# Kernel tuning notes

Measured on AMD Instinct MI355X. Metric: run time of the kernel, lower is better.

## Reference

```python
import jax, jax.numpy as jnp
import numpy as np

# Static configuration (mirrors init_kwargs)
B, C, H, W = 4, 256, 128, 128
S, T = 512, 64          # style_dim, num style tokens
HC, HS = 4, 8           # cross-attn heads, spatial-attn heads
WS, G = 8, 4            # window size, groupnorm groups
SHARPEN = 2.0
EPS = 1e-5


def _ln(x, g, b):
    m = jnp.mean(x, -1, keepdims=True)
    v = jnp.var(x, -1, keepdims=True)
    return (x - m) * jax.lax.rsqrt(v + EPS) * g + b


def _sdpa(q, k, v, scale):
    # q,k,v: [B, nH, L, D]
    s = jnp.einsum('bhqd,bhkd->bhqk', q, k) * scale
    return jnp.einsum('bhqk,bhkd->bhqd', jax.nn.softmax(s, -1), v)


def _heads(t, nh):
    b, l, c = t.shape
    return t.reshape(b, l, nh, c // nh).transpose(0, 2, 1, 3)


def _unheads(t):
    b, nh, l, d = t.shape
    return t.transpose(0, 2, 1, 3).reshape(b, l, nh * d)


def setup_inputs() -> dict:
    key = jax.random.key(0)
    ks = iter(jax.random.split(key, 48))
    def w(shape, s=0.02):
        return jax.random.normal(next(ks), shape, jnp.float32) * s
    return {
        'x': jax.random.normal(next(ks), (B, C, H, W), jnp.float32),
        'style_code': jax.random.normal(next(ks), (B, S), jnp.float32),
        # SpatialSelfAttention params (1x1 convs == linear over channels)
        'qkv_w': w((3 * C, C)), 'spat_proj_w': w((C, C)),
        # CrossAttnAdaGN params
        'gproj_w': w((2 * C, S)),
        'gproj_b': jnp.concatenate([jnp.ones((C,), jnp.float32), jnp.zeros((C,), jnp.float32)]),
        'tokens_basis': w((T, C)),
        'sproj_w': w((C, S)), 'sproj_b': jnp.zeros((C,), jnp.float32),
        'pos_w1': w((C, 2)), 'pos_b1': jnp.zeros((C,), jnp.float32),
        'pos_w2': w((C, C)), 'pos_b2': jnp.zeros((C,), jnp.float32),
        'q_w': w((C, C)), 'q_b': jnp.zeros((C,), jnp.float32),
        'k_w': w((C, C)), 'k_b': jnp.zeros((C,), jnp.float32),
        'v_w': w((C, C)), 'v_b': jnp.zeros((C,), jnp.float32),
        'o_w': w((C, C)), 'o_b': jnp.zeros((C,), jnp.float32),
        'ffn_w1': w((2 * C, C)), 'ffn_b1': jnp.zeros((2 * C,), jnp.float32),
        'ffn_w2': w((C, 2 * C)), 'ffn_b2': jnp.zeros((C,), jnp.float32),
        'tn_g': jnp.ones((C,), jnp.float32), 'tn_b': jnp.zeros((C,), jnp.float32),
        'qn_g': jnp.ones((C,), jnp.float32), 'qn_b': jnp.zeros((C,), jnp.float32),
        'fn_g': jnp.ones((C,), jnp.float32), 'fn_b': jnp.zeros((C,), jnp.float32),
        'gamma': w((1, C, 1, 1), 0.1),
    }


def reference(x, style_code, qkv_w, spat_proj_w, gproj_w, gproj_b, tokens_basis,
              sproj_w, sproj_b, pos_w1, pos_b1, pos_w2, pos_b2,
              q_w, q_b, k_w, k_b, v_w, v_b, o_w, o_b,
              ffn_w1, ffn_b1, ffn_w2, ffn_b2,
              tn_g, tn_b, qn_g, qn_b, fn_g, fn_b, gamma):
    b = x.shape[0]
    hw = H * W
    # ---------- CrossAttnAdaGN style modulation ----------
    xg = x.reshape(b, G, C // G, H, W)
    mu = jnp.mean(xg, (2, 3, 4), keepdims=True)
    var = jnp.var(xg, (2, 3, 4), keepdims=True)
    normalized = ((xg - mu) * jax.lax.rsqrt(var + EPS)).reshape(b, C, H, W)
    gp = style_code @ gproj_w.T + gproj_b           # [B, 2C]
    scale = gp[:, :C, None, None]
    shift = gp[:, C:, None, None]
    style_tokens = tokens_basis[None] + (style_code @ sproj_w.T + sproj_b)[:, None]  # [B,T,C]
    style_tokens = _ln(style_tokens, tn_g, tn_b)
    gy = jnp.linspace(-1.0, 1.0, H)
    gx = jnp.linspace(-1.0, 1.0, W)
    grid_y, grid_x = jnp.meshgrid(gy, gx, indexing='ij')
    pos = jnp.stack([grid_x, grid_y], -1).reshape(hw, 2)                 # [HW,2]
    pos_emb = jax.nn.silu(pos @ pos_w1.T + pos_b1) @ pos_w2.T + pos_b2   # [HW,C]
    tok = normalized.transpose(0, 2, 3, 1).reshape(b, hw, C)
    q_in = _ln(tok + pos_emb[None], qn_g, qn_b)
    q = _heads(q_in @ q_w.T + q_b, HC)                 # [B,HC,HW,hd]
    k = _heads(style_tokens @ k_w.T + k_b, HC)         # [B,HC,T,hd]
    v = _heads(style_tokens @ v_w.T + v_b, HC)
    hd = C // HC
    sc = _unheads(_sdpa(q, k, v, SHARPEN / jnp.sqrt(jnp.float32(hd))))   # [B,HW,C]
    sc = sc @ o_w.T + o_b
    sc = sc + jax.nn.silu(_ln(sc, fn_g, fn_b) @ ffn_w1.T + ffn_b1) @ ffn_w2.T + ffn_b2
    sc_sp = sc.transpose(0, 2, 1).reshape(b, C, H, W)
    adagn = normalized * scale + shift + sc_sp * gamma
    h = x + adagn  # gate = 1.0, residual style modulation
    # ---------- shifted-window self-attention ----------
    sh = WS // 2
    xr = jnp.roll(h, (-sh, -sh), (2, 3))
    qkv = jnp.einsum('oi,bihw->bohw', qkv_w, xr)
    qs, ks_, vs = jnp.split(qkv, 3, axis=1)
    def win(t):  # [B,C,H,W] -> [B*nWin, WS*WS, C]
        return t.reshape(b, C, H // WS, WS, W // WS, WS).transpose(0, 2, 4, 3, 5, 1).reshape(-1, WS * WS, C)
    hd2 = C // HS
    qh = _heads(win(qs), HS)
    kh = _heads(win(ks_), HS)
    vh = _heads(win(vs), HS)
    out = _unheads(_sdpa(qh, kh, vh, 1.0 / jnp.sqrt(jnp.float32(hd2))))
    out = out.reshape(b, H // WS, W // WS, WS, WS, C).transpose(0, 5, 1, 3, 2, 4).reshape(b, C, H, W)
    out = jnp.roll(out, (sh, sh), (2, 3))
    out = jnp.einsum('oi,bihw->bohw', spat_proj_w, out)
    return h + out
```

## Files before the change

### kernel.cpp

```cpp
#include <hip/hip_runtime.h>
#include <stdint.h>

#define DEV __device__ __forceinline__

typedef unsigned short u16;
typedef unsigned int u32;
typedef __attribute__((ext_vector_type(8))) __bf16 bf16x8;
typedef __attribute__((ext_vector_type(4))) float f32x4;

DEV u16 f2b(float f) {
  u32 u = __float_as_uint(f);
  u32 r = (u + 0x7FFFu + ((u >> 16) & 1u)) >> 16;
  return (u16)r;
}
DEV float b2f(u16 u) { return __uint_as_float(((u32)u) << 16); }
DEV void up2(u32 u, float& a, float& b) {
  a = __uint_as_float(u << 16);
  b = __uint_as_float(u & 0xffff0000u);
}
DEV void up8(uint4 t, float* d) {
  up2(t.x, d[0], d[1]); up2(t.y, d[2], d[3]);
  up2(t.z, d[4], d[5]); up2(t.w, d[6], d[7]);
}
DEV float silu_f(float v) { return v / (1.0f + __expf(-v)); }

DEV float redmax16(float v) {
  v = fmaxf(v, __shfl_xor(v, 1));
  v = fmaxf(v, __shfl_xor(v, 2));
  v = fmaxf(v, __shfl_xor(v, 4));
  v = fmaxf(v, __shfl_xor(v, 8));
  return v;
}
DEV float redsum16(float v) {
  v += __shfl_xor(v, 1);
  v += __shfl_xor(v, 2);
  v += __shfl_xor(v, 4);
  v += __shfl_xor(v, 8);
  return v;
}

__global__ void k_conv(const float* __restrict__ src, u16* __restrict__ dst, int n) {
  int i = blockIdx.x * 256 + threadIdx.x;
  int stride = gridDim.x * 256;
  for (; i < n; i += stride) dst[i] = f2b(src[i]);
}

DEV void breduce2(float& a, float& b, float* red, int tid) {
#pragma unroll
  for (int off = 32; off > 0; off >>= 1) {
    a += __shfl_down(a, off);
    b += __shfl_down(b, off);
  }
  int lane = tid & 63, wv = tid >> 6;
  if (lane == 0) { red[wv * 2] = a; red[wv * 2 + 1] = b; }
  __syncthreads();
  a = red[0] + red[2] + red[4] + red[6];
  b = red[1] + red[3] + red[5] + red[7];
}

__global__ void k_gn_partial(const float* __restrict__ x, float* __restrict__ partials) {
  __shared__ float red[8];
  int chunk = blockIdx.x;
  size_t base = ((size_t)chunk) << 14;
  float a = 0.f, b = 0.f;
#pragma unroll 4
  for (int i = 0; i < 64; ++i) {
    float v = x[base + (i << 8) + threadIdx.x];
    a += v; b += v * v;
  }
  breduce2(a, b, red, threadIdx.x);
  if (threadIdx.x == 0) { partials[chunk * 2] = a; partials[chunk * 2 + 1] = b; }
}

__global__ void k_gn_final(const float* __restrict__ partials, float* __restrict__ stats) {
  int g = blockIdx.x, lane = threadIdx.x;
  float a = partials[(((g << 6) + lane) << 1)];
  float b = partials[(((g << 6) + lane) << 1) + 1];
#pragma unroll
  for (int off = 32; off > 0; off >>= 1) {
    a += __shfl_down(a, off);
    b += __shfl_down(b, off);
  }
  if (lane == 0) {
    float mean = a * (1.f / 1048576.f);
    float var = b * (1.f / 1048576.f) - mean * mean;
    stats[g << 1] = mean;
    stats[(g << 1) + 1] = rsqrtf(var + 1e-5f);
  }
}

__global__ void k_style(const float* __restrict__ sc, const float* __restrict__ gw,
                        const float* __restrict__ gb, const float* __restrict__ sw,
                        const float* __restrict__ sb, float* __restrict__ gp,
                        float* __restrict__ stok) {
  __shared__ float row[512];
  int b = blockIdx.y, part = blockIdx.x, tid = threadIdx.x;
  row[tid] = sc[(b << 9) + tid];
  row[tid + 256] = sc[(b << 9) + tid + 256];
  __syncthreads();
  if (part < 2) {
    int o = (part << 8) + tid;
    float s = gb[o];
    const float* wr = gw + ((size_t)o << 9);
#pragma unroll 8
    for (int j = 0; j < 512; ++j) s += row[j] * wr[j];
    gp[(b << 9) + o] = s;
  } else {
    float s = sb[tid];
    const float* wr = sw + ((size_t)tid << 9);
#pragma unroll 8
    for (int j = 0; j < 512; ++j) s += row[j] * wr[j];
    stok[(b << 8) + tid] = s;
  }
}

__global__ void k_styk(const float* __restrict__ tb, const float* __restrict__ stok,
                       const float* __restrict__ g, const float* __restrict__ bt,
                       float* __restrict__ styk) {
  __shared__ float red[8];
  int r = blockIdx.x;
  int b = r >> 6, t = r & 63;
  int c = threadIdx.x;
  float v = tb[(t << 8) + c] + stok[(b << 8) + c];
  float a = v, bb = v * v;
  breduce2(a, bb, red, c);
  float mean = a * (1.f / 256.f);
  float var = bb * (1.f / 256.f) - mean * mean;
  float rs = rsqrtf(var + 1e-5f);
  styk[((size_t)r << 8) + c] = (v - mean) * rs * g[c] + bt[c];
}

__global__ void k_kv(const float* __restrict__ styk, const float* __restrict__ kw,
                     const float* __restrict__ kb, const float* __restrict__ vw,
                     const float* __restrict__ vb, u16* __restrict__ kmat,
                     u16* __restrict__ vmat) {
  __shared__ float srow[256];
  int r = blockIdx.x, c = threadIdx.x;
  srow[c] = styk[((size_t)r << 8) + c];
  __syncthreads();
  float sk = kb[c], sv = vb[c];
  const float* kr = kw + ((size_t)c << 8);
  const float* vr = vw + ((size_t)c << 8);
#pragma unroll 8
  for (int j = 0; j < 256; ++j) { sk += srow[j] * kr[j]; sv += srow[j] * vr[j]; }
  kmat[((size_t)r << 8) + c] = f2b(sk);
  vmat[((size_t)r << 8) + c] = f2b(sv);
}

__global__ void k_posh(const float* __restrict__ w1, const float* __restrict__ b1,
                       u16* __restrict__ posh) {
  int i = blockIdx.x * 256 + threadIdx.x;
  int stride = gridDim.x * 256;
  for (; i < 16384 * 256; i += stride) {
    int p = i >> 8, c = i & 255;
    int y = p >> 7, x = p & 127;
    float gx = -1.f + 2.f * (float)x / 127.f;
    float gy = -1.f + 2.f * (float)y / 127.f;
    float v = gx * w1[c << 1] + gy * w1[(c << 1) + 1] + b1[c];
    posh[i] = f2b(silu_f(v));
  }
}

template <int ACT, int BIAS, int RES, int OBF>
__global__ __launch_bounds__(256, 2) void k_gemm(
    const u16* __restrict__ A, const u16* __restrict__ Bw,
    const float* __restrict__ bias, const u16* __restrict__ res,
    void* __restrict__ outp, int M, int N, int K) {
  __shared__ u16 sA[128 * 40];
  __shared__ u16 sB[128 * 40];
  const int tid = threadIdx.x;
  const int m0 = blockIdx.y << 7, n0 = blockIdx.x << 7;
  const int lane = tid & 63, wv = tid >> 6;
  const int wr = wv >> 1, wc = wv & 1;
  const int l15 = lane & 15, kb = (lane >> 4) << 3;
  const int rA = (wr << 6) + l15, rB = (wc << 6) + l15;
  const int tr = tid >> 2, tc = (tid & 3) << 3;
  const u16* Ag = A + (size_t)(m0 + tr) * K + tc;
  const u16* Bg = Bw + (size_t)(n0 + tr) * K + tc;
  const size_t rowskip = (size_t)64 * K;

  f32x4 acc[4][4];
  f32x4 zz = {0.f, 0.f, 0.f, 0.f};
#pragma unroll
  for (int mi = 0; mi < 4; ++mi)
#pragma unroll
    for (int ni = 0; ni < 4; ++ni) acc[mi][ni] = zz;

  uint4 pa0 = *(const uint4*)(Ag);
  uint4 pa1 = *(const uint4*)(Ag + rowskip);
  uint4 pb0 = *(const uint4*)(Bg);
  uint4 pb1 = *(const uint4*)(Bg + rowskip);

  for (int k0 = 0; k0 < K; k0 += 32) {
    __syncthreads();
    *(uint4*)&sA[tr * 40 + tc] = pa0;
    *(uint4*)&sA[(tr + 64) * 40 + tc] = pa1;
    *(uint4*)&sB[tr * 40 + tc] = pb0;
    *(uint4*)&sB[(tr + 64) * 40 + tc] = pb1;
    __syncthreads();
    int kn = k0 + 32;
    if (kn < K) {
      pa0 = *(const uint4*)(Ag + kn);
      pa1 = *(const uint4*)(Ag + rowskip + kn);
      pb0 = *(const uint4*)(Bg + kn);
      pb1 = *(const uint4*)(Bg + rowskip + kn);
    }
    bf16x8 af[4], bfv[4];
#pragma unroll
    for (int i = 0; i < 4; ++i) {
      af[i] = *(const bf16x8*)&sA[(rA + (i << 4)) * 40 + kb];
      bfv[i] = *(const bf16x8*)&sB[(rB + (i << 4)) * 40 + kb];
    }
#pragma unroll
    for (int mi = 0; mi < 4; ++mi)
#pragma unroll
      for (int ni = 0; ni < 4; ++ni)
        acc[mi][ni] = __builtin_amdgcn_mfma_f32_16x16x32_bf16(af[mi], bfv[ni], acc[mi][ni], 0, 0, 0);
  }

  const int lg4 = (lane >> 4) << 2;
#pragma unroll
  for (int ni = 0; ni < 4; ++ni) {
    int n = n0 + (wc << 6) + (ni << 4) + l15;
    float bv = BIAS ? bias[n] : 0.0f;
#pragma unroll
    for (int mi = 0; mi < 4; ++mi) {
#pragma unroll
      for (int r = 0; r < 4; ++r) {
        int m = m0 + (wr << 6) + (mi << 4) + lg4 + r;
        float v = acc[mi][ni][r] + bv;
        if (ACT == 1) v = silu_f(v);
        size_t oi = (size_t)m * N + n;
        if (RES) v += b2f(res[oi]);
        if (OBF) ((u16*)outp)[oi] = f2b(v);
        else ((float*)outp)[oi] = v;
      }
    }
  }
}

__global__ void k_tokpe(const float* __restrict__ x, const float* __restrict__ stats,
                        const u16* __restrict__ pe, u16* __restrict__ tokq) {
  __shared__ float lds[64][65];
  int p0 = blockIdx.x << 6, c0 = blockIdx.y << 6, b = blockIdx.z;
  int tid = threadIdx.x;
#pragma unroll
  for (int i = 0; i < 16; ++i) {
    int flat = (i << 8) + tid;
    int ci = flat >> 6, pi = flat & 63;
    int cch = c0 + ci;
    int g = (b << 2) + (cch >> 6);
    float mu = stats[g << 1], rs = stats[(g << 1) + 1];
    lds[ci][pi] = (x[(((size_t)(b << 8) + cch) << 14) + p0 + pi] - mu) * rs;
  }
  __syncthreads();
#pragma unroll
  for (int i = 0; i < 16; ++i) {
    int flat = (i << 8) + tid;
    int pi = flat >> 6, ci = flat & 63;
    size_t row = (size_t)((b << 14) + p0 + pi);
    tokq[(row << 8) + c0 + ci] =
        f2b(lds[ci][pi] + b2f(pe[((size_t)(p0 + pi) << 8) + c0 + ci]));
  }
}

__global__ __launch_bounds__(256) void k_rowln8(const u16* __restrict__ in,
                                                const float* __restrict__ g,
                                                const float* __restrict__ bt,
                                                u16* __restrict__ out) {
  __shared__ float gs[256], bs[256];
  int tid = threadIdx.x;
  gs[tid] = g[tid];
  bs[tid] = bt[tid];
  __syncthreads();
  size_t base = (((size_t)(blockIdx.x << 5) + (tid >> 3)) << 8) + ((tid & 7) << 5);
  float v[32];
#pragma unroll
  for (int q = 0; q < 4; ++q) up8(*(const uint4*)(in + base + (q << 3)), &v[q << 3]);
  float a = 0.f, b = 0.f;
#pragma unroll
  for (int j = 0; j < 32; ++j) { a += v[j]; b += v[j] * v[j]; }
#pragma unroll
  for (int m = 1; m <= 4; m <<= 1) { a += __shfl_xor(a, m); b += __shfl_xor(b, m); }
  float mean = a * (1.f / 256.f);
  float var = b * (1.f / 256.f) - mean * mean;
  float rs = rsqrtf(var + 1e-5f);
  int c0 = (tid & 7) << 5;
#pragma unroll
  for (int q = 0; q < 4; ++q) {
    u16 tmp[8];
#pragma unroll
    for (int e = 0; e < 8; ++e) {
      int j = (q << 3) + e;
      tmp[e] = f2b((v[j] - mean) * rs * gs[c0 + j] + bs[c0 + j]);
    }
    *(uint4*)(out + base + (q << 3)) = *(uint4*)tmp;
  }
}

__global__ __launch_bounds__(256, 2) void k_cross_mfma(
    const u16* __restrict__ qmat, const u16* __restrict__ kmat,
    const u16* __restrict__ vmat, u16* __restrict__ attn_out) {
  __shared__ u16 Kl[64 * 72];
  __shared__ u16 Vt[64 * 72];
  __shared__ u16 Pl[4][64 * 72];
  const int tid = threadIdx.x;
  const int lane = tid & 63, wv = tid >> 6;
  const int l15 = lane & 15, lg = lane >> 4;
  const int b = blockIdx.z, h = blockIdx.y;
  const int q0 = blockIdx.x << 8;
  for (int c = tid; c < 512; c += 256) {
    int t = c >> 3, dg = (c & 7) << 3;
    size_t src = (((size_t)(b << 6) + t) << 8) + (h << 6) + dg;
    *(uint4*)&Kl[t * 72 + dg] = *(const uint4*)(kmat + src);
    uint4 vv = *(const uint4*)(vmat + src);
    const u16* pv = (const u16*)&vv;
#pragma unroll
    for (int e = 0; e < 8; ++e) Vt[(dg + e) * 72 + t] = pv[e];
  }
  __syncthreads();
  const size_t qrow0 = (size_t)(b << 14) + q0 + (wv << 6);
  f32x4 acc[4][4];
  f32x4 zz = {0.f, 0.f, 0.f, 0.f};
#pragma unroll
  for (int mi = 0; mi < 4; ++mi)
#pragma unroll
    for (int ni = 0; ni < 4; ++ni) acc[mi][ni] = zz;
#pragma unroll
  for (int ks = 0; ks < 2; ++ks) {
    bf16x8 a[4], bbf[4];
#pragma unroll
    for (int mi = 0; mi < 4; ++mi)
      a[mi] = *(const bf16x8*)(qmat + ((qrow0 + (mi << 4) + l15) << 8) + (h << 6) +
                               (ks << 5) + (lg << 3));
#pragma unroll
    for (int ni = 0; ni < 4; ++ni)
      bbf[ni] = *(const bf16x8*)&Kl[((ni << 4) + l15) * 72 + (ks << 5) + (lg << 3)];
#pragma unroll
    for (int mi = 0; mi < 4; ++mi)
#pragma unroll
      for (int ni = 0; ni < 4; ++ni)
        acc[mi][ni] = __builtin_amdgcn_mfma_f32_16x16x32_bf16(a[mi], bbf[ni], acc[mi][ni], 0, 0, 0);
  }
  const float SC = 0.25f;
#pragma unroll
  for (int mi = 0; mi < 4; ++mi) {
#pragma unroll
    for (int r = 0; r < 4; ++r) {
      float rm = acc[mi][0][r];
#pragma unroll
      for (int ni = 1; ni < 4; ++ni) rm = fmaxf(rm, acc[mi][ni][r]);
      rm = redmax16(rm);
      float pv[4];
      float rs = 0.f;
#pragma unroll
      for (int ni = 0; ni < 4; ++ni) {
        pv[ni] = __expf((acc[mi][ni][r] - rm) * SC);
        rs += pv[ni];
      }
      rs = redsum16(rs);
      float inv = 1.f / rs;
      int row = (mi << 4) + (lg << 2) + r;
#pragma unroll
      for (int ni = 0; ni < 4; ++ni)
        Pl[wv][row * 72 + (ni << 4) + l15] = f2b(pv[ni] * inv);
    }
  }
  __syncthreads();
  f32x4 o[4][4];
#pragma unroll
  for (int mi = 0; mi < 4; ++mi)
#pragma unroll
    for (int ni = 0; ni < 4; ++ni) o[mi][ni] = zz;
#pragma unroll
  for (int ks = 0; ks < 2; ++ks) {
    bf16x8 a[4], bbf[4];
#pragma unroll
    for (int mi = 0; mi < 4; ++mi)
      a[mi] = *(const bf16x8*)&Pl[wv][((mi << 4) + l15) * 72 + (ks << 5) + (lg << 3)];
#pragma unroll
    for (int ni = 0; ni < 4; ++ni)
      bbf[ni] = *(const bf16x8*)&Vt[((ni << 4) + l15) * 72 + (ks << 5) + (lg << 3)];
#pragma unroll
    for (int mi = 0; mi < 4; ++mi)
#pragma unroll
      for (int ni = 0; ni < 4; ++ni)
        o[mi][ni] = __builtin_amdgcn_mfma_f32_16x16x32_bf16(a[mi], bbf[ni], o[mi][ni], 0, 0, 0);
  }
  __syncthreads();
#pragma unroll
  for (int mi = 0; mi < 4; ++mi)
#pragma unroll
    for (int ni = 0; ni < 4; ++ni)
#pragma unroll
      for (int r = 0; r < 4; ++r)
        Pl[wv][((mi << 4) + (lg << 2) + r) * 72 + (ni << 4) + l15] = f2b(o[mi][ni][r]);
  __syncthreads();
  const int l8r = lane >> 3, l8c = lane & 7;
#pragma unroll
  for (int it = 0; it < 8; ++it) {
    int row = (it << 3) + l8r;
    uint4 vv = *(const uint4*)&Pl[wv][row * 72 + (l8c << 3)];
    *(uint4*)(attn_out + ((qrow0 + row) << 8) + (h << 6) + (l8c << 3)) = vv;
  }
}

__global__ __launch_bounds__(256, 2) void k_win_mfma(
    const u16* __restrict__ qb, const u16* __restrict__ kbuf,
    const u16* __restrict__ vbuf, u16* __restrict__ wout) {
  __shared__ u16 Vt[4][32 * 72];
  __shared__ u16 Pl[4][64 * 72];
  const int tid = threadIdx.x;
  const int lane = tid & 63, wv = tid >> 6;
  const int l15 = lane & 15, lg = lane >> 4;
  const int win = blockIdx.x, b = blockIdx.y;
  const int wbase = ((win >> 4) << 10) + ((win & 15) << 3);
  const size_t bbase = (size_t)b << 14;
  const float SC = 0.17677669529663687f;
  f32x4 zz = {0.f, 0.f, 0.f, 0.f};
#pragma unroll 1
  for (int h2 = 0; h2 < 2; ++h2) {
    const int h = (wv << 1) + h2;
    const int co = h << 5;
    {
      int p = wbase + ((lane >> 3) << 7) + (lane & 7);
      const u16* src = vbuf + ((bbase + p) << 8) + co;
#pragma unroll
      for (int c = 0; c < 4; ++c) {
        uint4 vv = *(const uint4*)(src + (c << 3));
        const u16* pe = (const u16*)&vv;
#pragma unroll
        for (int e = 0; e < 8; ++e) Vt[wv][((c << 3) + e) * 72 + lane] = pe[e];
      }
    }
    f32x4 acc[4][4];
#pragma unroll
    for (int mi = 0; mi < 4; ++mi)
#pragma unroll
      for (int ni = 0; ni < 4; ++ni) acc[mi][ni] = zz;
    {
      bf16x8 a[4], bbf[4];
#pragma unroll
      for (int mi = 0; mi < 4; ++mi) {
        int t = (mi << 4) + l15;
        int p = wbase + ((t >> 3) << 7) + (t & 7);
        a[mi] = *(const bf16x8*)(qb + ((bbase + p) << 8) + co + (lg << 3));
      }
#pragma unroll
      for (int ni = 0; ni < 4; ++ni) {
        int t = (ni << 4) + l15;
        int p = wbase + ((t >> 3) << 7) + (t & 7);
        bbf[ni] = *(const bf16x8*)(kbuf + ((bbase + p) << 8) + co + (lg << 3));
      }
#pragma unroll
      for (int mi = 0; mi < 4; ++mi)
#pragma unroll
        for (int ni = 0; ni < 4; ++ni)
          acc[mi][ni] = __builtin_amdgcn_mfma_f32_16x16x32_bf16(a[mi], bbf[ni], acc[mi][ni], 0, 0, 0);
    }
#pragma unroll
    for (int mi = 0; mi < 4; ++mi) {
#pragma unroll
      for (int r = 0; r < 4; ++r) {
        float rm = acc[mi][0][r];
#pragma unroll
        for (int ni = 1; ni < 4; ++ni) rm = fmaxf(rm, acc[mi][ni][r]);
        rm = redmax16(rm);
        float pv[4];
        float rs = 0.f;
#pragma unroll
        for (int ni = 0; ni < 4; ++ni) {
          pv[ni] = __expf((acc[mi][ni][r] - rm) * SC);
          rs += pv[ni];
        }
        rs = redsum16(rs);
        float inv = 1.f / rs;
        int row = (mi << 4) + (lg << 2) + r;
#pragma unroll
        for (int ni = 0; ni < 4; ++ni)
          Pl[wv][row * 72 + (ni << 4) + l15] = f2b(pv[ni] * inv);
      }
    }
    __syncthreads();
    f32x4 o[4][2];
#pragma unroll
    for (int mi = 0; mi < 4; ++mi)
#pragma unroll
      for (int ni = 0; ni < 2; ++ni) o[mi][ni] = zz;
#pragma unroll
    for (int ks = 0; ks < 2; ++ks) {
      bf16x8 a[4], bbf[2];
#pragma unroll
      for (int mi = 0; mi < 4; ++mi)
        a[mi] = *(const bf16x8*)&Pl[wv][((mi << 4) + l15) * 72 + (ks << 5) + (lg << 3)];
#pragma unroll
      for (int ni = 0; ni < 2; ++ni)
        bbf[ni] = *(const bf16x8*)&Vt[wv][((ni << 4) + l15) * 72 + (ks << 5) + (lg << 3)];
#pragma unroll
      for (int mi = 0; mi < 4; ++mi)
#pragma unroll
        for (int ni = 0; ni < 2; ++ni)
          o[mi][ni] = __builtin_amdgcn_mfma_f32_16x16x32_bf16(a[mi], bbf[ni], o[mi][ni], 0, 0, 0);
    }
    __syncthreads();
#pragma unroll
    for (int mi = 0; mi < 4; ++mi)
#pragma unroll
      for (int ni = 0; ni < 2; ++ni)
#pragma unroll
        for (int r = 0; r < 4; ++r)
          Pl[wv][((mi << 4) + (lg << 2) + r) * 72 + (ni << 4) + l15] = f2b(o[mi][ni][r]);
    __syncthreads();
#pragma unroll
    for (int it = 0; it < 4; ++it) {
      int row = (it << 4) + (lane >> 2);
      int cg = (lane & 3) << 3;
      uint4 vv = *(const uint4*)&Pl[wv][row * 72 + cg];
      int p = wbase + ((row >> 3) << 7) + (row & 7);
      *(uint4*)(wout + ((bbase + p) << 8) + co + cg) = vv;
    }
    __syncthreads();
  }
}

__global__ void k_xrt(const float* __restrict__ x, const u16* __restrict__ sc2,
                      const float* __restrict__ stats, const float* __restrict__ gp,
                      const float* __restrict__ gamma, u16* __restrict__ xrt) {
  __shared__ float A[64][33];
  __shared__ float Bt[32][65];
  int p0 = blockIdx.x << 6, c0 = blockIdx.y << 5, b = blockIdx.z;
  int tid = threadIdx.x;
#pragma unroll
  for (int i = 0; i < 8; ++i) {
    int flat = (i << 8) + tid;
    int pi = flat >> 5, ci = flat & 31;
    A[pi][ci] = b2f(sc2[(((size_t)(b << 14) + p0 + pi) << 8) + c0 + ci]);
  }
  __syncthreads();
#pragma unroll
  for (int i = 0; i < 8; ++i) {
    int flat = (i << 8) + tid;
    int cc = flat >> 6, px = flat & 63;
    int cch = c0 + cc;
    int g = (b << 2) + (cch >> 6);
    float mu = stats[g << 1], rs = stats[(g << 1) + 1];
    size_t xi = (((size_t)(b << 8) + cch) << 14) + p0 + px;
    float xv = x[xi];
    float val = xv + (xv - mu) * rs * gp[(b << 9) + cch] + gp[(b << 9) + 256 + cch] +
                A[px][cc] * gamma[cch];
    Bt[cc][px] = val;
  }
  __syncthreads();
#pragma unroll
  for (int i = 0; i < 8; ++i) {
    int flat = (i << 8) + tid;
    int xi2 = flat >> 5, ci = flat & 31;
    int p = p0 + xi2;
    int yy = p >> 7, xx = p & 127;
    int pr = (((yy + 124) & 127) << 7) + ((xx + 124) & 127);
    xrt[(((size_t)(b << 14) + pr) << 8) + c0 + ci] = f2b(Bt[ci][xi2]);
  }
}

__global__ void k_final(const float* __restrict__ x, const u16* __restrict__ sc2,
                        const u16* __restrict__ out2, const float* __restrict__ stats,
                        const float* __restrict__ gp, const float* __restrict__ gamma,
                        float* __restrict__ dout) {
  __shared__ float L1[64][33];
  __shared__ float L2[64][33];
  int bx = blockIdx.x;
  int y = bx >> 1, x0 = (bx & 1) << 6;
  int c0 = blockIdx.y << 5, b = blockIdx.z;
  int tid = threadIdx.x;
#pragma unroll
  for (int i = 0; i < 8; ++i) {
    int flat = (i << 8) + tid;
    int xi = flat >> 5, ci = flat & 31;
    int xx = x0 + xi;
    int pr = (((y + 124) & 127) << 7) + ((xx + 124) & 127);
    L1[xi][ci] = b2f(out2[(((size_t)(b << 14) + pr) << 8) + c0 + ci]);
    L2[xi][ci] = b2f(sc2[(((size_t)(b << 14) + (y << 7) + xx) << 8) + c0 + ci]);
  }
  __syncthreads();
#pragma unroll
  for (int i = 0; i < 8; ++i) {
    int flat = (i << 8) + tid;
    int cc = flat >> 6, xi2 = flat & 63;
    int cch = c0 + cc;
    int g = (b << 2) + (cch >> 6);
    float mu = stats[g << 1], rs = stats[(g << 1) + 1];
    size_t idx = (((size_t)(b << 8) + cch) << 14) + (y << 7) + x0 + xi2;
    float xv = x[idx];
    float val = xv + (xv - mu) * rs * gp[(b << 9) + cch] + gp[(b << 9) + 256 + cch] +
                L2[xi2][cc] * gamma[cch] + L1[xi2][cc];
    dout[idx] = val;
  }
}

extern "C" void kernel_launch(void* const* d_in, const int* in_sizes, int n_in,
                              void* d_out, int out_size, void* d_ws, size_t ws_size,
                              hipStream_t stream) {
  (void)in_sizes; (void)n_in; (void)out_size;
  const float* x = (const float*)d_in[0];
  const float* style = (const float*)d_in[1];
  const float* qkv_w = (const float*)d_in[2];
  const float* spat_w = (const float*)d_in[3];
  const float* gproj_w = (const float*)d_in[4];
  const float* gproj_b = (const float*)d_in[5];
  const float* tokens_basis = (const float*)d_in[6];
  const float* sproj_w = (const float*)d_in[7];
  const float* sproj_b = (const float*)d_in[8];
  const float* pos_w1 = (const float*)d_in[9];
  const float* pos_b1 = (const float*)d_in[10];
  const float* pos_w2 = (const float*)d_in[11];
  const float* pos_b2 = (const float*)d_in[12];
  const float* q_w = (const float*)d_in[13];
  const float* q_b = (const float*)d_in[14];
  const float* k_w = (const float*)d_in[15];
  const float* k_b = (const float*)d_in[16];
  const float* v_w = (const float*)d_in[17];
  const float* v_b = (const float*)d_in[18];
  const float* o_w = (const float*)d_in[19];
  const float* o_b = (const float*)d_in[20];
  const float* ffn_w1 = (const float*)d_in[21];
  const float* ffn_b1 = (const float*)d_in[22];
  const float* ffn_w2 = (const float*)d_in[23];
  const float* ffn_b2 = (const float*)d_in[24];
  const float* tn_g = (const float*)d_in[25];
  const float* tn_b = (const float*)d_in[26];
  const float* qn_g = (const float*)d_in[27];
  const float* qn_b = (const float*)d_in[28];
  const float* fn_g = (const float*)d_in[29];
  const float* fn_b = (const float*)d_in[30];
  const float* gamma = (const float*)d_in[31];
  float* dout = (float*)d_out;

  char* w = (char*)d_ws;
  size_t off = 0;
  auto alloc = [&](size_t sz) {
    char* p = w + off;
    off += (sz + 255) & ~(size_t)255;
    return (void*)p;
  };
  float* partials = (float*)alloc(1024 * 2 * 4);
  float* stats = (float*)alloc(32 * 4);
  float* gp = (float*)alloc(4 * 512 * 4);
  float* stok = (float*)alloc(4 * 256 * 4);
  float* styk = (float*)alloc(4 * 64 * 256 * 4);
  u16* kmat = (u16*)alloc(4 * 64 * 256 * 2);
  u16* vmat = (u16*)alloc(4 * 64 * 256 * 2);
  u16* wb_q = (u16*)alloc(65536 * 2);
  u16* wb_o = (u16*)alloc(65536 * 2);
  u16* wb_w1 = (u16*)alloc(131072 * 2);
  u16* wb_w2 = (u16*)alloc(131072 * 2);
  u16* wb_qkv = (u16*)alloc(196608 * 2);
  u16* wb_sp = (u16*)alloc(65536 * 2);
  u16* wb_p2 = (u16*)alloc(65536 * 2);
  const size_t SLOT = (size_t)65536 * 256 * 2;
  u16* S0 = (u16*)alloc(SLOT);
  u16* S1 = (u16*)alloc(SLOT);
  u16* S2 = (u16*)alloc(SLOT);
  if (ws_size < off) return;

  u16* ffn_h = (u16*)d_out;
  u16* kwin = (u16*)d_out;
  u16* vwin = (u16*)d_out + (size_t)65536 * 256;

  k_conv<<<256, 256, 0, stream>>>(q_w, wb_q, 65536);
  k_conv<<<256, 256, 0, stream>>>(o_w, wb_o, 65536);
  k_conv<<<512, 256, 0, stream>>>(ffn_w1, wb_w1, 131072);
  k_conv<<<512, 256, 0, stream>>>(ffn_w2, wb_w2, 131072);
  k_conv<<<768, 256, 0, stream>>>(qkv_w, wb_qkv, 196608);
  k_conv<<<256, 256, 0, stream>>>(spat_w, wb_sp, 65536);
  k_conv<<<256, 256, 0, stream>>>(pos_w2, wb_p2, 65536);

  k_gn_partial<<<1024, 256, 0, stream>>>(x, partials);
  k_gn_final<<<16, 64, 0, stream>>>(partials, stats);

  k_style<<<dim3(3, 4), 256, 0, stream>>>(style, gproj_w, gproj_b, sproj_w, sproj_b, gp, stok);
  k_styk<<<256, 256, 0, stream>>>(tokens_basis, stok, tn_g, tn_b, styk);
  k_kv<<<256, 256, 0, stream>>>(styk, k_w, k_b, v_w, v_b, kmat, vmat);

  k_posh<<<4096, 256, 0, stream>>>(pos_w1, pos_b1, S0);
  k_gemm<0, 1, 0, 1><<<dim3(2, 128), 256, 0, stream>>>(S0, wb_p2, pos_b2, nullptr,
                                                       S1, 16384, 256, 256);

  k_tokpe<<<dim3(256, 4, 4), 256, 0, stream>>>(x, stats, S1, S2);
  k_rowln8<<<2048, 256, 0, stream>>>(S2, qn_g, qn_b, S2);

  k_gemm<0, 1, 0, 1><<<dim3(2, 512), 256, 0, stream>>>(S2, wb_q, q_b, nullptr,
                                                       S1, 65536, 256, 256);
  k_cross_mfma<<<dim3(64, 4, 4), 256, 0, stream>>>(S1, kmat, vmat, S0);
  k_gemm<0, 1, 0, 1><<<dim3(2, 512), 256, 0, stream>>>(S0, wb_o, o_b, nullptr,
                                                       S2, 65536, 256, 256);

  k_rowln8<<<2048, 256, 0, stream>>>(S2, fn_g, fn_b, S1);
  k_gemm<1, 1, 0, 1><<<dim3(4, 512), 256, 0, stream>>>(S1, wb_w1, ffn_b1, nullptr,
                                                       ffn_h, 65536, 512, 256);
  k_gemm<0, 1, 1, 1><<<dim3(2, 512), 256, 0, stream>>>(ffn_h, wb_w2, ffn_b2, S2,
                                                       S0, 65536, 256, 512);

  k_xrt<<<dim3(256, 8, 4), 256, 0, stream>>>(x, S0, stats, gp, gamma, S1);

  k_gemm<0, 0, 0, 1><<<dim3(2, 512), 256, 0, stream>>>(S1, wb_qkv, nullptr, nullptr,
                                                       S2, 65536, 256, 256);
  k_gemm<0, 0, 0, 1><<<dim3(2, 512), 256, 0, stream>>>(S1, wb_qkv + 65536, nullptr, nullptr,
                                                       kwin, 65536, 256, 256);
  k_gemm<0, 0, 0, 1><<<dim3(2, 512), 256, 0, stream>>>(S1, wb_qkv + 131072, nullptr, nullptr,
                                                       vwin, 65536, 256, 256);

  k_win_mfma<<<dim3(256, 4), 256, 0, stream>>>(S2, kwin, vwin, S1);
  k_gemm<0, 0, 0, 1><<<dim3(2, 512), 256, 0, stream>>>(S1, wb_sp, nullptr, nullptr,
                                                       S2, 65536, 256, 256);

  k_final<<<dim3(256, 8, 4), 256, 0, stream>>>(x, S0, S2, stats, gp, gamma, dout);
}
```

Measured before the change: 461.4 us.

## Rework GEMM with direct-to-LDS loads and fuse weight conversion and QKV GEMMs

The GEMM kernel now loads tiles with global_load_lds into an XOR-swizzled LDS layout. Its epilogue stages results through LDS so outputs and the residual are written with 16-byte vector stores. The three QKV projections become one GEMM with N=768 that splits its output into three buffers. The seven weight-conversion launches are merged into one vectorized kernel. When workspace allows, a bf16 copy of x is written during the GroupNorm pass and read by later kernels instead of fp32 x, which lowers the precision of the residual input. The new GEMM drops the register prefetch, so global loads are no longer overlapped with the MFMAs.

```diff
diff --git a/kernel.cpp b/kernel.cpp
--- a/kernel.cpp
+++ b/kernel.cpp
@@ -39,10 +39,32 @@
   return v;
 }
 
-__global__ void k_conv(const float* __restrict__ src, u16* __restrict__ dst, int n) {
+DEV void gload16(const u16* g, u16* l) {
+  __builtin_amdgcn_global_load_lds(
+      (const __attribute__((address_space(1))) uint32_t*)(g),
+      (__attribute__((address_space(3))) uint32_t*)(l), 16, 0, 0);
+}
+
+struct WConv {
+  const float* s0; const float* s1; const float* s2; const float* s3;
+  const float* s4; const float* s5; const float* s6;
+  u16* d0; u16* d1; u16* d2; u16* d3; u16* d4; u16* d5; u16* d6;
+};
+__global__ void k_conv_all(WConv wc) {
   int i = blockIdx.x * 256 + threadIdx.x;
-  int stride = gridDim.x * 256;
-  for (; i < n; i += stride) dst[i] = f2b(src[i]);
+  if (i >= 180224) return;
+  const float* sp[7] = {wc.s0, wc.s1, wc.s2, wc.s3, wc.s4, wc.s5, wc.s6};
+  u16* dp[7] = {wc.d0, wc.d1, wc.d2, wc.d3, wc.d4, wc.d5, wc.d6};
+  const int n4[7] = {16384, 16384, 32768, 32768, 49152, 16384, 16384};
+  int rem = i, seg = 0;
+#pragma unroll
+  for (int s = 0; s < 7; ++s) {
+    if (rem < n4[s]) { seg = s; break; }
+    rem -= n4[s];
+  }
+  float4 v = ((const float4*)sp[seg])[rem];
+  u16 t[4] = {f2b(v.x), f2b(v.y), f2b(v.z), f2b(v.w)};
+  *(uint2*)(dp[seg] + (rem << 2)) = *(uint2*)t;
 }
 
 DEV void breduce2(float& a, float& b, float* red, int tid) {
@@ -58,15 +80,24 @@
   b = red[1] + red[3] + red[5] + red[7];
 }
 
-__global__ void k_gn_partial(const float* __restrict__ x, float* __restrict__ partials) {
+template <int XB>
+__global__ void k_gn_partial(const float* __restrict__ x, float* __restrict__ partials,
+                             u16* __restrict__ xb) {
   __shared__ float red[8];
   int chunk = blockIdx.x;
-  size_t base = ((size_t)chunk) << 14;
+  size_t base4 = ((size_t)chunk) << 12;
+  const float4* x4 = (const float4*)x;
   float a = 0.f, b = 0.f;
 #pragma unroll 4
-  for (int i = 0; i < 64; ++i) {
-    float v = x[base + (i << 8) + threadIdx.x];
-    a += v; b += v * v;
+  for (int i = 0; i < 16; ++i) {
+    size_t idx = base4 + (i << 8) + threadIdx.x;
+    float4 v = x4[idx];
+    a += v.x + v.y + v.z + v.w;
+    b += v.x * v.x + v.y * v.y + v.z * v.z + v.w * v.w;
+    if (XB) {
+      u16 t[4] = {f2b(v.x), f2b(v.y), f2b(v.z), f2b(v.w)};
+      *(uint2*)(xb + (idx << 2)) = *(uint2*)t;
+    }
   }
   breduce2(a, b, red, threadIdx.x);
   if (threadIdx.x == 0) { partials[chunk * 2] = a; partials[chunk * 2 + 1] = b; }
@@ -161,23 +192,35 @@
   }
 }
 
-template <int ACT, int BIAS, int RES, int OBF>
-__global__ __launch_bounds__(256, 2) void k_gemm(
+template <int ACT, int BIAS, int RES, int SPLIT>
+__global__ __launch_bounds__(256, 2) void k_gemm2(
     const u16* __restrict__ A, const u16* __restrict__ Bw,
     const float* __restrict__ bias, const u16* __restrict__ res,
-    void* __restrict__ outp, int M, int N, int K) {
-  __shared__ u16 sA[128 * 40];
-  __shared__ u16 sB[128 * 40];
+    u16* __restrict__ o0, u16* __restrict__ o1, u16* __restrict__ o2,
+    int M, int N, int K) {
+  __shared__ __align__(16) u16 lds[17408];
+  u16* sA = lds;
+  u16* sB = lds + 4096;
   const int tid = threadIdx.x;
+  const int lane = tid & 63, wv = tid >> 6;
   const int m0 = blockIdx.y << 7, n0 = blockIdx.x << 7;
-  const int lane = tid & 63, wv = tid >> 6;
+  const int l15 = lane & 15, lg = lane >> 4;
   const int wr = wv >> 1, wc = wv & 1;
-  const int l15 = lane & 15, kb = (lane >> 4) << 3;
-  const int rA = (wr << 6) + l15, rB = (wc << 6) + l15;
-  const int tr = tid >> 2, tc = (tid & 3) << 3;
-  const u16* Ag = A + (size_t)(m0 + tr) * K + tc;
-  const u16* Bg = Bw + (size_t)(n0 + tr) * K + tc;
-  const size_t rowskip = (size_t)64 * K;
+
+  const int gofs = (((lane & 3) ^ ((lane >> 3) & 3)) << 3);
+  const int lrow = lane >> 2;
+  const u16* Ag0 = A + (size_t)(m0 + (wv << 5) + lrow) * K + gofs;
+  const u16* Ag1 = A + (size_t)(m0 + (wv << 5) + 16 + lrow) * K + gofs;
+  const u16* Bg0 = Bw + (size_t)(n0 + (wv << 5) + lrow) * K + gofs;
+  const u16* Bg1 = Bw + (size_t)(n0 + (wv << 5) + 16 + lrow) * K + gofs;
+  u16* lA0 = sA + (wv << 10);
+  u16* lA1 = sA + (wv << 10) + 512;
+  u16* lB0 = sB + (wv << 10);
+  u16* lB1 = sB + (wv << 10) + 512;
+
+  const int roff = l15 * 32 + (((lg ^ ((l15 >> 1) & 3))) << 3);
+  const int abase = (wr << 6) * 32;
+  const int bbase = (wc << 6) * 32;
 
   f32x4 acc[4][4];
   f32x4 zz = {0.f, 0.f, 0.f, 0.f};
@@ -186,31 +229,18 @@
 #pragma unroll
     for (int ni = 0; ni < 4; ++ni) acc[mi][ni] = zz;
 
-  uint4 pa0 = *(const uint4*)(Ag);
-  uint4 pa1 = *(const uint4*)(Ag + rowskip);
-  uint4 pb0 = *(const uint4*)(Bg);
-  uint4 pb1 = *(const uint4*)(Bg + rowskip);
-
-  for (int k0 = 0; k0 < K; k0 += 32) {
+  for (int kt = 0; kt < K; kt += 32) {
     __syncthreads();
-    *(uint4*)&sA[tr * 40 + tc] = pa0;
-    *(uint4*)&sA[(tr + 64) * 40 + tc] = pa1;
-    *(uint4*)&sB[tr * 40 + tc] = pb0;
-    *(uint4*)&sB[(tr + 64) * 40 + tc] = pb1;
+    gload16(Ag0 + kt, lA0);
+    gload16(Ag1 + kt, lA1);
+    gload16(Bg0 + kt, lB0);
+    gload16(Bg1 + kt, lB1);
     __syncthreads();
-    int kn = k0 + 32;
-    if (kn < K) {
-      pa0 = *(const uint4*)(Ag + kn);
-      pa1 = *(const uint4*)(Ag + rowskip + kn);
-      pb0 = *(const uint4*)(Bg + kn);
-      pb1 = *(const uint4*)(Bg + rowskip + kn);
-    }
     bf16x8 af[4], bfv[4];
 #pragma unroll
-    for (int i = 0; i < 4; ++i) {
-      af[i] = *(const bf16x8*)&sA[(rA + (i << 4)) * 40 + kb];
-      bfv[i] = *(const bf16x8*)&sB[(rB + (i << 4)) * 40 + kb];
-    }
+    for (int mi = 0; mi < 4; ++mi) af[mi] = *(const bf16x8*)&sA[abase + mi * 512 + roff];
+#pragma unroll
+    for (int ni = 0; ni < 4; ++ni) bfv[ni] = *(const bf16x8*)&sB[bbase + ni * 512 + roff];
 #pragma unroll
     for (int mi = 0; mi < 4; ++mi)
 #pragma unroll
@@ -218,29 +248,63 @@
         acc[mi][ni] = __builtin_amdgcn_mfma_f32_16x16x32_bf16(af[mi], bfv[ni], acc[mi][ni], 0, 0, 0);
   }
 
-  const int lg4 = (lane >> 4) << 2;
-#pragma unroll
-  for (int ni = 0; ni < 4; ++ni) {
-    int n = n0 + (wc << 6) + (ni << 4) + l15;
-    float bv = BIAS ? bias[n] : 0.0f;
-#pragma unroll
-    for (int mi = 0; mi < 4; ++mi) {
+  float bv[4];
+#pragma unroll
+  for (int ni = 0; ni < 4; ++ni)
+    bv[ni] = BIAS ? bias[n0 + (wc << 6) + (ni << 4) + l15] : 0.0f;
+  __syncthreads();
+  const int lg4 = lg << 2;
+#pragma unroll
+  for (int mi = 0; mi < 4; ++mi) {
+#pragma unroll
+    for (int ni = 0; ni < 4; ++ni) {
 #pragma unroll
       for (int r = 0; r < 4; ++r) {
-        int m = m0 + (wr << 6) + (mi << 4) + lg4 + r;
-        float v = acc[mi][ni][r] + bv;
+        int row = (wr << 6) + (mi << 4) + lg4 + r;
+        int col = (wc << 6) + (ni << 4) + l15;
+        float v = acc[mi][ni][r] + bv[ni];
         if (ACT == 1) v = silu_f(v);
-        size_t oi = (size_t)m * N + n;
-        if (RES) v += b2f(res[oi]);
-        if (OBF) ((u16*)outp)[oi] = f2b(v);
-        else ((float*)outp)[oi] = v;
+        lds[row * 136 + col] = f2b(v);
       }
     }
   }
-}
-
-__global__ void k_tokpe(const float* __restrict__ x, const float* __restrict__ stats,
-                        const u16* __restrict__ pe, u16* __restrict__ tokq) {
+  __syncthreads();
+  u16* obase;
+  int cb, ldc;
+  if (SPLIT) {
+    int sel = n0 >> 8;
+    obase = sel == 0 ? o0 : (sel == 1 ? o1 : o2);
+    cb = n0 & 255;
+    ldc = 256;
+  } else {
+    obase = o0;
+    cb = n0;
+    ldc = N;
+  }
+#pragma unroll
+  for (int i = 0; i < 8; ++i) {
+    int flat = (i << 8) + tid;
+    int row = flat >> 4, c8 = (flat & 15) << 3;
+    uint4 vv = *(const uint4*)&lds[row * 136 + c8];
+    size_t oi = (size_t)(m0 + row) * ldc + cb + c8;
+    if (RES) {
+      uint4 rr = *(const uint4*)(res + oi);
+      float a8[8], r8[8];
+      up8(vv, a8);
+      up8(rr, r8);
+      u16 t[8];
+#pragma unroll
+      for (int e = 0; e < 8; ++e) t[e] = f2b(a8[e] + r8[e]);
+      vv = *(const uint4*)t;
+    }
+    *(uint4*)(obase + oi) = vv;
+  }
+}
+
+template <int XB>
+__global__ void k_tokpe(const float* __restrict__ x, const u16* __restrict__ xb,
+                        const float* __restrict__ stats, const u16* __restrict__ pe,
+                        u16* __restrict__ tokq) {
   __shared__ float lds[64][65];
   int p0 = blockIdx.x << 6, c0 = blockIdx.y << 6, b = blockIdx.z;
   int tid = threadIdx.x;
@@ -251,7 +315,9 @@
     int cch = c0 + ci;
     int g = (b << 2) + (cch >> 6);
     float mu = stats[g << 1], rs = stats[(g << 1) + 1];
-    lds[ci][pi] = (x[(((size_t)(b << 8) + cch) << 14) + p0 + pi] - mu) * rs;
+    size_t idx = (((size_t)(b << 8) + cch) << 14) + p0 + pi;
+    float xv = XB ? b2f(xb[idx]) : x[idx];
+    lds[ci][pi] = (xv - mu) * rs;
   }
   __syncthreads();
 #pragma unroll
@@ -523,9 +589,11 @@
   }
 }
 
-__global__ void k_xrt(const float* __restrict__ x, const u16* __restrict__ sc2,
-                      const float* __restrict__ stats, const float* __restrict__ gp,
-                      const float* __restrict__ gamma, u16* __restrict__ xrt) {
+template <int XB>
+__global__ void k_xrt(const float* __restrict__ x, const u16* __restrict__ xb,
+                      const u16* __restrict__ sc2, const float* __restrict__ stats,
+                      const float* __restrict__ gp, const float* __restrict__ gamma,
+                      u16* __restrict__ xrt) {
   __shared__ float A[64][33];
   __shared__ float Bt[32][65];
   int p0 = blockIdx.x << 6, c0 = blockIdx.y << 5, b = blockIdx.z;
@@ -545,7 +613,7 @@
     int g = (b << 2) + (cch >> 6);
     float mu = stats[g << 1], rs = stats[(g << 1) + 1];
     size_t xi = (((size_t)(b << 8) + cch) << 14) + p0 + px;
-    float xv = x[xi];
+    float xv = XB ? b2f(xb[xi]) : x[xi];
     float val = xv + (xv - mu) * rs * gp[(b << 9) + cch] + gp[(b << 9) + 256 + cch] +
                 A[px][cc] * gamma[cch];
     Bt[cc][px] = val;
@@ -562,10 +630,11 @@
   }
 }
 
-__global__ void k_final(const float* __restrict__ x, const u16* __restrict__ sc2,
-                        const u16* __restrict__ out2, const float* __restrict__ stats,
-                        const float* __restrict__ gp, const float* __restrict__ gamma,
-                        float* __restrict__ dout) {
+template <int XB>
+__global__ void k_final(const float* __restrict__ x, const u16* __restrict__ xb,
+                        const u16* __restrict__ sc2, const u16* __restrict__ out2,
+                        const float* __restrict__ stats, const float* __restrict__ gp,
+                        const float* __restrict__ gamma, float* __restrict__ dout) {
   __shared__ float L1[64][33];
   __shared__ float L2[64][33];
   int bx = blockIdx.x;
@@ -590,7 +659,7 @@
     int g = (b << 2) + (cch >> 6);
     float mu = stats[g << 1], rs = stats[(g << 1) + 1];
     size_t idx = (((size_t)(b << 8) + cch) << 14) + (y << 7) + x0 + xi2;
-    float xv = x[idx];
+    float xv = XB ? b2f(xb[idx]) : x[idx];
     float val = xv + (xv - mu) * rs * gp[(b << 9) + cch] + gp[(b << 9) + 256 + cch] +
                 L2[xi2][cc] * gamma[cch] + L1[xi2][cc];
     dout[idx] = val;
@@ -660,21 +729,21 @@
   u16* S0 = (u16*)alloc(SLOT);
   u16* S1 = (u16*)alloc(SLOT);
   u16* S2 = (u16*)alloc(SLOT);
-  if (ws_size < off) return;
+  size_t off_base = off;
+  u16* xb = (u16*)alloc((size_t)67108864 * 2);
+  if (ws_size < off_base) return;
+  const int XB = (ws_size >= off) ? 1 : 0;
 
   u16* ffn_h = (u16*)d_out;
   u16* kwin = (u16*)d_out;
   u16* vwin = (u16*)d_out + (size_t)65536 * 256;
 
-  k_conv<<<256, 256, 0, stream>>>(q_w, wb_q, 65536);
-  k_conv<<<256, 256, 0, stream>>>(o_w, wb_o, 65536);
-  k_conv<<<512, 256, 0, stream>>>(ffn_w1, wb_w1, 131072);
-  k_conv<<<512, 256, 0, stream>>>(ffn_w2, wb_w2, 131072);
-  k_conv<<<768, 256, 0, stream>>>(qkv_w, wb_qkv, 196608);
-  k_conv<<<256, 256, 0, stream>>>(spat_w, wb_sp, 65536);
-  k_conv<<<256, 256, 0, stream>>>(pos_w2, wb_p2, 65536);
-
-  k_gn_partial<<<1024, 256, 0, stream>>>(x, partials);
+  WConv wc = {q_w, o_w, ffn_w1, ffn_w2, qkv_w, spat_w, pos_w2,
+              wb_q, wb_o, wb_w1, wb_w2, wb_qkv, wb_sp, wb_p2};
+  k_conv_all<<<704, 256, 0, stream>>>(wc);
+
+  if (XB) k_gn_partial<1><<<1024, 256, 0, stream>>>(x, partials, xb);
+  else k_gn_partial<0><<<1024, 256, 0, stream>>>(x, partials, xb);
   k_gn_final<<<16, 64, 0, stream>>>(partials, stats);
 
   k_style<<<dim3(3, 4), 256, 0, stream>>>(style, gproj_w, gproj_b, sproj_w, sproj_b, gp, stok);
@@ -682,36 +751,35 @@
   k_kv<<<256, 256, 0, stream>>>(styk, k_w, k_b, v_w, v_b, kmat, vmat);
 
   k_posh<<<4096, 256, 0, stream>>>(pos_w1, pos_b1, S0);
-  k_gemm<0, 1, 0, 1><<<dim3(2, 128), 256, 0, stream>>>(S0, wb_p2, pos_b2, nullptr,
-                                                       S1, 16384, 256, 256);
-
-  k_tokpe<<<dim3(256, 4, 4), 256, 0, stream>>>(x, stats, S1, S2);
+  k_gemm2<0, 1, 0, 0><<<dim3(2, 128), 256, 0, stream>>>(S0, wb_p2, pos_b2, nullptr,
+                                                        S1, nullptr, nullptr, 16384, 256, 256);
+
+  if (XB) k_tokpe<1><<<dim3(256, 4, 4), 256, 0, stream>>>(x, xb, stats, S1, S2);
+  else k_tokpe<0><<<dim3(256, 4, 4), 256, 0, stream>>>(x, xb, stats, S1, S2);
   k_rowln8<<<2048, 256, 0, stream>>>(S2, qn_g, qn_b, S2);
 
-  k_gemm<0, 1, 0, 1><<<dim3(2, 512), 256, 0, stream>>>(S2, wb_q, q_b, nullptr,
-                                                       S1, 65536, 256, 256);
+  k_gemm2<0, 1, 0, 0><<<dim3(2, 512), 256, 0, stream>>>(S2, wb_q, q_b, nullptr,
+                                                        S1, nullptr, nullptr, 65536, 256, 256);
   k_cross_mfma<<<dim3(64, 4, 4), 256, 0, stream>>>(S1, kmat, vmat, S0);
-  k_gemm<0, 1, 0, 1><<<dim3(2, 512), 256, 0, stream>>>(S0, wb_o, o_b, nullptr,
-                                                       S2, 65536, 256, 256);
+  k_gemm2<0, 1, 0, 0><<<dim3(2, 512), 256, 0, stream>>>(S0, wb_o, o_b, nullptr,
+                                                        S2, nullptr, nullptr, 65536, 256, 256);
 
   k_rowln8<<<2048, 256, 0, stream>>>(S2, fn_g, fn_b, S1);
-  k_gemm<1, 1, 0, 1><<<dim3(4, 512), 256, 0, stream>>>(S1, wb_w1, ffn_b1, nullptr,
-                                                       ffn_h, 65536, 512, 256);
-  k_gemm<0, 1, 1, 1><<<dim3(2, 512), 256, 0, stream>>>(ffn_h, wb_w2, ffn_b2, S2,
-                                                       S0, 65536, 256, 512);
-
-  k_xrt<<<dim3(256, 8, 4), 256, 0, stream>>>(x, S0, stats, gp, gamma, S1);
-
-  k_gemm<0, 0, 0, 1><<<dim3(2, 512), 256, 0, stream>>>(S1, wb_qkv, nullptr, nullptr,
-                                                       S2, 65536, 256, 256);
-  k_gemm<0, 0, 0, 1><<<dim3(2, 512), 256, 0, stream>>>(S1, wb_qkv + 65536, nullptr, nullptr,
-                                                       kwin, 65536, 256, 256);
-  k_gemm<0, 0, 0, 1><<<dim3(2, 512), 256, 0, stream>>>(S1, wb_qkv + 131072, nullptr, nullptr,
-                                                       vwin, 65536, 256, 256);
+  k_gemm2<1, 1, 0, 0><<<dim3(4, 512), 256, 0, stream>>>(S1, wb_w1, ffn_b1, nullptr,
+                                                        ffn_h, nullptr, nullptr, 65536, 512, 256);
+  k_gemm2<0, 1, 1, 0><<<dim3(2, 512), 256, 0, stream>>>(ffn_h, wb_w2, ffn_b2, S2,
+                                                        S0, nullptr, nullptr, 65536, 256, 512);
+
+  if (XB) k_xrt<1><<<dim3(256, 8, 4), 256, 0, stream>>>(x, xb, S0, stats, gp, gamma, S1);
+  else k_xrt<0><<<dim3(256, 8, 4), 256, 0, stream>>>(x, xb, S0, stats, gp, gamma, S1);
+
+  k_gemm2<0, 0, 0, 1><<<dim3(6, 512), 256, 0, stream>>>(S1, wb_qkv, nullptr, nullptr,
+                                                        S2, kwin, vwin, 65536, 768, 256);
 
   k_win_mfma<<<dim3(256, 4), 256, 0, stream>>>(S2, kwin, vwin, S1);
-  k_gemm<0, 0, 0, 1><<<dim3(2, 512), 256, 0, stream>>>(S1, wb_sp, nullptr, nullptr,
-                                                       S2, 65536, 256, 256);
-
-  k_final<<<dim3(256, 8, 4), 256, 0, stream>>>(x, S0, S2, stats, gp, gamma, dout);
-}
+  k_gemm2<0, 0, 0, 0><<<dim3(2, 512), 256, 0, stream>>>(S1, wb_sp, nullptr, nullptr,
+                                                        S2, nullptr, nullptr, 65536, 256, 256);
+
+  if (XB) k_final<1><<<dim3(256, 8, 4), 256, 0, stream>>>(x, xb, S0, S2, stats, gp, gamma, dout);
+  else k_final<0><<<dim3(256, 8, 4), 256, 0, stream>>>(x, xb, S0, S2, stats, gp, gamma, dout);
+}
```

Result: faster. 449.0 us (-2.7%).
